# Optimization experiments

Measured on AMD Instinct MI355X. Metric: run time of the kernel, lower is better.

Reference implementation:

```python
import jax, jax.numpy as jnp
import numpy as np

B, F, N = 16, 64, 32768
C0, C1, C2 = 64, 16, 1
TOP_K = 64
EPS = 1e-5


def setup_inputs() -> dict:
    key = jax.random.key(0)
    ks = jax.random.split(key, 6)
    def rn(k, shape, scale=1.0):
        return jax.random.normal(k, shape, dtype=jnp.float32) * scale
    return {
        "sortvec": rn(ks[0], (B, 1, F, N)),
        "input": rn(ks[1], (B, F, N)),
        # conv0: kernel (F,1), in=1, out=64 -> weight reduces to [C0, F]
        "w0": rn(ks[2], (C0, F), np.sqrt(2.0 / F)), "b0": jnp.zeros((C0,), jnp.float32),
        "w1": rn(ks[3], (C1, C0), np.sqrt(2.0 / C0)), "b1": jnp.zeros((C1,), jnp.float32),
        "w2": rn(ks[4], (C2, C1), np.sqrt(2.0 / C1)), "b2": jnp.zeros((C2,), jnp.float32),
        "g0": jnp.ones((C0,), jnp.float32), "bt0": jnp.zeros((C0,), jnp.float32),
        "g1": jnp.ones((C1,), jnp.float32), "bt1": jnp.zeros((C1,), jnp.float32),
        "g2": jnp.ones((C2,), jnp.float32), "bt2": jnp.zeros((C2,), jnp.float32),
    }


def _bn_relu(x, g, b):
    # training-mode BatchNorm2d over (B, N) per channel; x: [B, C, N]
    mu = jnp.mean(x, axis=(0, 2), keepdims=True)
    var = jnp.var(x, axis=(0, 2), keepdims=True)
    return jax.nn.relu((x - mu) * jax.lax.rsqrt(var + EPS) * g[None, :, None] + b[None, :, None])


def reference(sortvec, input, w0, b0, w1, b1, w2, b2, g0, bt0, g1, bt1, g2, bt2):
    # conv0 with kernel (F,1) collapses the feature axis: [B,1,F,N] -> [B,C0,N]
    x = jnp.einsum('bfn,of->bon', sortvec[:, 0], w0) + b0[None, :, None]
    x = _bn_relu(x, g0, bt0)
    x = _bn_relu(jnp.einsum('bcn,oc->bon', x, w1) + b1[None, :, None], g1, bt1)
    score = _bn_relu(jnp.einsum('bcn,oc->bon', x, w2) + b2[None, :, None], g2, bt2)  # [B,1,N]
    _, idx = jax.lax.top_k(score[:, 0], TOP_K)                                        # [B,K]
    sorted_input = jnp.take_along_axis(input, idx[:, None, :], axis=2)                # [B,F,K]
    sorted_score = jnp.take_along_axis(score, idx[:, None, :], axis=2)                # [B,1,K]
    feat = jnp.concatenate([sorted_input, sorted_score], axis=1)                      # [B,F+1,K]
    return feat, idx
```

## Files before the change

### kernel.cpp

```cpp
#include <hip/hip_runtime.h>


constexpr int   B_   = 16;
constexpr int   N_   = 32768;
constexpr int   K_   = 64;
constexpr long long S_ = (long long)B_ * N_;
constexpr float EPS_ = 1e-5f;

constexpr int T128  = 4096;
constexpr int NB0   = 2048;
constexpr int NB1   = 2048;
constexpr int NB2   = 256;
constexpr int NBC   = 128;
constexpr int NBINS = 4096;
constexpr int CAP   = 1024;

__device__ __forceinline__ unsigned key_map(float f) {
  unsigned u = __float_as_uint(f);
  return (u & 0x80000000u) ? ~u : (u | 0x80000000u);
}

__global__ __launch_bounds__(256) void k_prep(const float* __restrict__ w0,
                                              const float* __restrict__ w1,
                                              float* __restrict__ w0T,
                                              float* __restrict__ w1T) {
  int t = threadIdx.x;
  for (int e = t; e < 64 * 64; e += 256) {
    int o = e >> 6, f = e & 63;
    w0T[f * 64 + o] = w0[e];
  }
  for (int e = t; e < 16 * 64; e += 256) {
    int o = e >> 6, c = e & 63;
    w1T[c * 16 + o] = w1[e];
  }
}

__global__ __launch_bounds__(256) void k_stat0(const float* __restrict__ sv,
                                               const float* __restrict__ w0T,
                                               const float* __restrict__ b0,
                                               float* __restrict__ p0) {
  __shared__ float svt[64][128];
  const int t  = threadIdx.x;
  const int p  = t & 63;
  const int cg = __builtin_amdgcn_readfirstlane(t >> 6);

  float bb[16];
#pragma unroll
  for (int j = 0; j < 16; ++j) bb[j] = b0[cg * 16 + j];

  float s1[16], s2[16];
#pragma unroll
  for (int j = 0; j < 16; ++j) { s1[j] = 0.f; s2[j] = 0.f; }

  for (int tile = blockIdx.x; tile < T128; tile += NB0) {
    const int b  = tile >> 8;
    const int n0 = (tile & 255) << 7;
    const float* src = sv + ((long long)b * 64) * N_ + n0;
    __syncthreads();
#pragma unroll
    for (int q = 0; q < 8; ++q) {
      int e = t + q * 256;
      int f = e >> 5, c4 = (e & 31) << 2;
      *(float4*)&svt[f][c4] = *(const float4*)(src + (long long)f * N_ + c4);
    }
    __syncthreads();

    float2 y[16];
#pragma unroll
    for (int j = 0; j < 16; ++j) { y[j].x = bb[j]; y[j].y = bb[j]; }
    for (int f = 0; f < 64; ++f) {
      const float2 x = *(const float2*)&svt[f][p << 1];
      const float* wr = w0T + f * 64 + cg * 16;
#pragma unroll
      for (int j = 0; j < 16; ++j) {
        y[j].x = fmaf(wr[j], x.x, y[j].x);
        y[j].y = fmaf(wr[j], x.y, y[j].y);
      }
    }
#pragma unroll
    for (int j = 0; j < 16; ++j) {
      s1[j] += y[j].x + y[j].y;
      s2[j] = fmaf(y[j].x, y[j].x, fmaf(y[j].y, y[j].y, s2[j]));
    }
  }

#pragma unroll
  for (int j = 0; j < 16; ++j) {
#pragma unroll
    for (int off = 32; off; off >>= 1) {
      s1[j] += __shfl_down(s1[j], off, 64);
      s2[j] += __shfl_down(s2[j], off, 64);
    }
  }
  if (p == 0) {
    float* dst = p0 + (long long)blockIdx.x * 128;
#pragma unroll
    for (int j = 0; j < 16; ++j) {
      dst[cg * 16 + j]      = s1[j];
      dst[64 + cg * 16 + j] = s2[j];
    }
  }
}

__global__ __launch_bounds__(1024) void k_reduce0(const float* __restrict__ p0,
                                                  const float* __restrict__ g,
                                                  const float* __restrict__ bt,
                                                  float* __restrict__ st) {
  __shared__ float l[8][128];
  const int t = threadIdx.x;
  const int j = t & 127, grp = t >> 7;
  float a0 = 0.f, a1 = 0.f, a2 = 0.f, a3 = 0.f;
  for (int i = grp; i < 512; i += 8) {
    a0 += p0[(long long)i * 128 + j];
    a1 += p0[(long long)(i + 512) * 128 + j];
    a2 += p0[(long long)(i + 1024) * 128 + j];
    a3 += p0[(long long)(i + 1536) * 128 + j];
  }
  l[grp][j] = (a0 + a1) + (a2 + a3);
  __syncthreads();
  if (t < 128) {
    float v = ((l[0][t] + l[1][t]) + (l[2][t] + l[3][t])) +
              ((l[4][t] + l[5][t]) + (l[6][t] + l[7][t]));
    l[0][t] = v;
  }
  __syncthreads();
  if (t < 64) {
    const float inv = 1.f / (float)S_;
    float mean = l[0][t] * inv;
    float ex2  = l[0][64 + t] * inv;
    float var  = ex2 - mean * mean;
    float sc   = g[t] * rsqrtf(var + EPS_);
    st[t]      = sc;
    st[64 + t] = bt[t] - mean * sc;
  }
}

__global__ __launch_bounds__(256) void k_layer01(const float* __restrict__ sv,
                                                 const float* __restrict__ w0T,
                                                 const float* __restrict__ b0,
                                                 const float* __restrict__ st0,
                                                 const float* __restrict__ w1T,
                                                 const float* __restrict__ b1,
                                                 float* __restrict__ y1,
                                                 float* __restrict__ p1) {
  __shared__ float buf[64][128];
  const int t  = threadIdx.x;
  const int p  = t & 63;
  const int cg = __builtin_amdgcn_readfirstlane(t >> 6);

  float bb[16], sc[16], sh[16];
#pragma unroll
  for (int j = 0; j < 16; ++j) {
    bb[j] = b0[cg * 16 + j];
    sc[j] = st0[cg * 16 + j];
    sh[j] = st0[64 + cg * 16 + j];
  }
  float bb1[4];
#pragma unroll
  for (int j = 0; j < 4; ++j) bb1[j] = b1[cg * 4 + j];

  float sA[4], qA[4];
#pragma unroll
  for (int j = 0; j < 4; ++j) { sA[j] = 0.f; qA[j] = 0.f; }

  for (int tile = blockIdx.x; tile < T128; tile += NB1) {
    const int b  = tile >> 8;
    const int n0 = (tile & 255) << 7;
    const float* src = sv + ((long long)b * 64) * N_ + n0;
    __syncthreads();
#pragma unroll
    for (int q = 0; q < 8; ++q) {
      int e = t + q * 256;
      int f = e >> 5, c4 = (e & 31) << 2;
      *(float4*)&buf[f][c4] = *(const float4*)(src + (long long)f * N_ + c4);
    }
    __syncthreads();

    float2 y[16];
#pragma unroll
    for (int j = 0; j < 16; ++j) { y[j].x = bb[j]; y[j].y = bb[j]; }
    for (int f = 0; f < 64; ++f) {
      const float2 x = *(const float2*)&buf[f][p << 1];
      const float* wr = w0T + f * 64 + cg * 16;
#pragma unroll
      for (int j = 0; j < 16; ++j) {
        y[j].x = fmaf(wr[j], x.x, y[j].x);
        y[j].y = fmaf(wr[j], x.y, y[j].y);
      }
    }
    __syncthreads();

#pragma unroll
    for (int j = 0; j < 16; ++j) {
      float2 h;
      h.x = fmaf(y[j].x, sc[j], sh[j]); h.x = h.x > 0.f ? h.x : 0.f;
      h.y = fmaf(y[j].y, sc[j], sh[j]); h.y = h.y > 0.f ? h.y : 0.f;
      *(float2*)&buf[cg * 16 + j][p << 1] = h;
    }
    __syncthreads();

    float2 z[4];
#pragma unroll
    for (int j = 0; j < 4; ++j) { z[j].x = bb1[j]; z[j].y = bb1[j]; }
    for (int c = 0; c < 64; ++c) {
      const float2 h = *(const float2*)&buf[c][p << 1];
      const float* wr = w1T + c * 16 + cg * 4;
#pragma unroll
      for (int j = 0; j < 4; ++j) {
        z[j].x = fmaf(wr[j], h.x, z[j].x);
        z[j].y = fmaf(wr[j], h.y, z[j].y);
      }
    }

    float* yo = y1 + ((long long)(b * 16 + cg * 4)) * N_ + n0 + (p << 1);
#pragma unroll
    for (int j = 0; j < 4; ++j) {
      *(float2*)(yo + (long long)j * N_) = z[j];
      sA[j] += z[j].x + z[j].y;
      qA[j] = fmaf(z[j].x, z[j].x, fmaf(z[j].y, z[j].y, qA[j]));
    }
  }

#pragma unroll
  for (int j = 0; j < 4; ++j) {
#pragma unroll
    for (int off = 32; off; off >>= 1) {
      sA[j] += __shfl_down(sA[j], off, 64);
      qA[j] += __shfl_down(qA[j], off, 64);
    }
  }
  if (p == 0) {
    float* dst = p1 + (long long)blockIdx.x * 32;
#pragma unroll
    for (int j = 0; j < 4; ++j) {
      dst[cg * 4 + j]      = sA[j];
      dst[16 + cg * 4 + j] = qA[j];
    }
  }
}

__global__ __launch_bounds__(1024) void k_reduce1(const float* __restrict__ p1,
                                                  const float* __restrict__ g,
                                                  const float* __restrict__ bt,
                                                  float* __restrict__ st) {
  __shared__ float l[32][32];
  const int t = threadIdx.x;
  const int j = t & 31, grp = t >> 5;
  float a0 = 0.f, a1 = 0.f;
  for (int i = grp; i < 1024; i += 32) {
    a0 += p1[(long long)i * 32 + j];
    a1 += p1[(long long)(i + 1024) * 32 + j];
  }
  l[grp][j] = a0 + a1;
  __syncthreads();
  if (t < 32) {
    float v = 0.f;
#pragma unroll
    for (int g2 = 0; g2 < 32; ++g2) v += l[g2][t];
    l[0][t] = v;
  }
  __syncthreads();
  if (t < 16) {
    const float inv = 1.f / (float)S_;
    float mean = l[0][t] * inv;
    float ex2  = l[0][16 + t] * inv;
    float var  = ex2 - mean * mean;
    float sc   = g[t] * rsqrtf(var + EPS_);
    st[t]      = sc;
    st[16 + t] = bt[t] - mean * sc;
  }
}

__global__ __launch_bounds__(1024) void k_layer2(const float* __restrict__ y1,
                                                 const float* __restrict__ st1,
                                                 const float* __restrict__ w2,
                                                 const float* __restrict__ b2,
                                                 float* __restrict__ y2,
                                                 float* __restrict__ p2,
                                                 int* __restrict__ ghist) {
  __shared__ int hist[NBINS];
  __shared__ float ls[16], lq[16];
  const int t   = threadIdx.x;
  const int blk = blockIdx.x;
  const int b   = blk >> 4;
  const int n0  = ((blk & 15) << 11) | (t << 1);

#pragma unroll
  for (int i = 0; i < NBINS / 1024; ++i) hist[t + i * 1024] = 0;

  float sc[16], sh[16], w[16];
#pragma unroll
  for (int c = 0; c < 16; ++c) { sc[c] = st1[c]; sh[c] = st1[16 + c]; w[c] = w2[c]; }
  const float bias = b2[0];

  float a0 = bias, a1 = bias;
  const float* base = y1 + ((long long)b * 16) * N_ + n0;
#pragma unroll
  for (int c = 0; c < 16; ++c) {
    float2 v = *(const float2*)(base + (long long)c * N_);
    float h;
    h = fmaf(v.x, sc[c], sh[c]); h = h > 0.f ? h : 0.f; a0 = fmaf(w[c], h, a0);
    h = fmaf(v.y, sc[c], sh[c]); h = h > 0.f ? h : 0.f; a1 = fmaf(w[c], h, a1);
  }
  float2 o; o.x = a0; o.y = a1;
  *(float2*)(y2 + (long long)b * N_ + n0) = o;

  __syncthreads();

  atomicAdd(&hist[key_map(a0) >> 20], 1);
  atomicAdd(&hist[key_map(a1) >> 20], 1);

  float ss = a0 + a1;
  float sq = fmaf(a0, a0, a1 * a1);
#pragma unroll
  for (int off = 32; off; off >>= 1) {
    ss += __shfl_down(ss, off, 64);
    sq += __shfl_down(sq, off, 64);
  }
  const int wid = t >> 6, lid = t & 63;
  if (lid == 0) { ls[wid] = ss; lq[wid] = sq; }
  __syncthreads();
  if (t == 0) {
    float Sv = 0.f, Qv = 0.f;
#pragma unroll
    for (int i = 0; i < 16; ++i) { Sv += ls[i]; Qv += lq[i]; }
    p2[blk * 2 + 0] = Sv;
    p2[blk * 2 + 1] = Qv;
  }
#pragma unroll
  for (int i = 0; i < NBINS / 1024; ++i) {
    int v = hist[t + i * 1024];
    if (v) atomicAdd(&ghist[b * NBINS + t + i * 1024], v);
  }
}

__global__ __launch_bounds__(256) void k_thresh(const int* __restrict__ ghist,
                                                int* __restrict__ Tb) {
  __shared__ int hl[NBINS + NBINS / 64];
  const int t = threadIdx.x, b = blockIdx.x;
  const int* h = ghist + b * NBINS;
  for (int i = t; i < NBINS; i += 256) hl[i + (i >> 6)] = h[i];
  __syncthreads();
  if (t < 64) {
    const int l = t;
    int s = 0;
    for (int j = 0; j < 64; ++j) s += hl[(l * 64 + j) + l];
    int Sv = s;
#pragma unroll
    for (int off = 1; off < 64; off <<= 1) {
      int v = __shfl_down(Sv, off, 64);
      if (l + off < 64) Sv += v;
    }
    unsigned long long m = __ballot(Sv >= K_);
    const int lstar = 63 - __builtin_clzll(m);
    const int tailS = (lstar < 63) ? __shfl(Sv, lstar + 1, 64) : 0;
    int Tj = hl[(lstar * 64 + l) + lstar];
#pragma unroll
    for (int off = 1; off < 64; off <<= 1) {
      int v = __shfl_down(Tj, off, 64);
      if (l + off < 64) Tj += v;
    }
    const int cge = Tj + tailS;
    unsigned long long m2 = __ballot(cge >= K_);
    const int jstar = 63 - __builtin_clzll(m2);
    if (l == 0) Tb[b] = lstar * 64 + jstar;
  }
}

__global__ __launch_bounds__(1024) void k_compact(const float* __restrict__ y2,
                                                  const int* __restrict__ Tb,
                                                  int* __restrict__ cnt,
                                                  unsigned long long* __restrict__ cand) {
  const int t = threadIdx.x, blk = blockIdx.x;
  const int b  = blk >> 3;
  const int n0 = ((blk & 7) << 12) | (t << 2);
  const int T  = Tb[b];
  float4 v = *(const float4*)(y2 + (long long)b * N_ + n0);
  unsigned long long* cb = cand + (long long)b * CAP;
#define DO_CAND(comp, off)                                                    \
  {                                                                           \
    unsigned u = key_map(comp);                                               \
    if ((int)(u >> 20) >= T) {                                                \
      int slot = atomicAdd(&cnt[b], 1);                                       \
      if (slot < CAP)                                                         \
        cb[slot] = ((unsigned long long)u << 32) |                            \
                   (unsigned)(N_ - 1 - (n0 + off));                           \
    }                                                                         \
  }
  DO_CAND(v.x, 0) DO_CAND(v.y, 1) DO_CAND(v.z, 2) DO_CAND(v.w, 3)
#undef DO_CAND
}

__global__ __launch_bounds__(64) void k_final(const unsigned long long* __restrict__ cand,
                                              const int* __restrict__ cnt,
                                              const float* __restrict__ p2,
                                              const float* __restrict__ g2,
                                              const float* __restrict__ bt2,
                                              const float* __restrict__ inp,
                                              float* __restrict__ out) {
  const int b = blockIdx.x, l = threadIdx.x;

  float s1 = (p2[2 * l] + p2[2 * (l + 64)]) +
             (p2[2 * (l + 128)] + p2[2 * (l + 192)]);
  float q1 = (p2[2 * l + 1] + p2[2 * (l + 64) + 1]) +
             (p2[2 * (l + 128) + 1] + p2[2 * (l + 192) + 1]);
#pragma unroll
  for (int off = 32; off; off >>= 1) {
    s1 += __shfl_down(s1, off, 64);
    q1 += __shfl_down(q1, off, 64);
  }
  s1 = __shfl(s1, 0, 64);
  q1 = __shfl(q1, 0, 64);
  const float inv = 1.f / (float)S_;
  const float mean = s1 * inv;
  const float var  = q1 * inv - mean * mean;
  const float scale2 = g2[0] * rsqrtf(var + EPS_);
  const float shift2 = bt2[0] - mean * scale2;

  int cn = cnt[b];
  if (cn > CAP) cn = CAP;
  const unsigned long long* cb = cand + (long long)b * CAP;
  unsigned long long k[16];
#pragma unroll
  for (int r = 0; r < 16; ++r) {
    int i = l + r * 64;
    k[r] = (i < cn) ? cb[i] : 0ull;
  }
  unsigned long long cur = 0ull;
#pragma unroll
  for (int r = 0; r < 16; ++r) cur = k[r] > cur ? k[r] : cur;

  int myidx = 0;
  unsigned mymap = 0;
  for (int r = 0; r < K_; ++r) {
    unsigned long long m = cur;
#pragma unroll
    for (int off = 32; off; off >>= 1) {
      unsigned long long o = __shfl_xor(m, off, 64);
      m = o > m ? o : m;
    }
    if (r == l) {
      myidx = N_ - 1 - (int)(m & 0xffffffffu);
      mymap = (unsigned)(m >> 32);
    }
    if (cur == m) {
#pragma unroll
      for (int r2 = 0; r2 < 16; ++r2)
        if (k[r2] == m) k[r2] = 0ull;
      unsigned long long c2 = 0ull;
#pragma unroll
      for (int r2 = 0; r2 < 16; ++r2) c2 = k[r2] > c2 ? k[r2] : c2;
      cur = c2;
    }
  }

  unsigned u = mymap;
  u = (u & 0x80000000u) ? (u & 0x7fffffffu) : ~u;
  float v = __uint_as_float(u);
  float scv = fmaf(v, scale2, shift2);
  scv = scv > 0.f ? scv : 0.f;

  const float* ib = inp + ((long long)b * 64) * N_;
#pragma unroll 4
  for (int f = 0; f < 64; ++f)
    out[((long long)b * 65 + f) * 64 + l] = ib[(long long)f * N_ + myidx];
  out[((long long)b * 65 + 64) * 64 + l] = scv;
  out[(long long)B_ * 65 * 64 + b * 64 + l] = (float)myidx;
}

extern "C" void kernel_launch(void* const* d_in, const int* in_sizes, int n_in,
                              void* d_out, int out_size, void* d_ws, size_t ws_size,
                              hipStream_t stream) {
  const float* sv  = (const float*)d_in[0];
  const float* inp = (const float*)d_in[1];
  const float* w0  = (const float*)d_in[2];
  const float* b0  = (const float*)d_in[3];
  const float* w1  = (const float*)d_in[4];
  const float* b1  = (const float*)d_in[5];
  const float* w2  = (const float*)d_in[6];
  const float* b2  = (const float*)d_in[7];
  const float* g0  = (const float*)d_in[8];
  const float* bt0 = (const float*)d_in[9];
  const float* g1  = (const float*)d_in[10];
  const float* bt1 = (const float*)d_in[11];
  const float* g2  = (const float*)d_in[12];
  const float* bt2 = (const float*)d_in[13];
  float* out = (float*)d_out;

  float* ws  = (float*)d_ws;
  float* y1  = ws;
  float* y2  = y1 + (size_t)S_ * 16;
  float* p0  = y2 + (size_t)S_;
  float* p1  = p0 + (size_t)NB0 * 128;
  float* p2  = p1 + (size_t)NB1 * 32;
  float* st0 = p2 + (size_t)NB2 * 2;
  float* st1 = st0 + 128;
  float* w0T = st1 + 32;
  float* w1T = w0T + 4096;
  int*   ghist = (int*)(w1T + 1024);
  int*   cnt   = ghist + (size_t)B_ * NBINS;
  int*   Tb    = cnt + 16;
  unsigned long long* cand =
      (unsigned long long*)(Tb + 16);

  hipMemsetAsync(ghist, 0, ((size_t)B_ * NBINS + 16) * sizeof(int), stream);

  k_prep   <<<1,    256, 0, stream>>>(w0, w1, w0T, w1T);
  k_stat0  <<<NB0,  256, 0, stream>>>(sv, w0T, b0, p0);
  k_reduce0<<<1,   1024, 0, stream>>>(p0, g0, bt0, st0);
  k_layer01<<<NB1,  256, 0, stream>>>(sv, w0T, b0, st0, w1T, b1, y1, p1);
  k_reduce1<<<1,   1024, 0, stream>>>(p1, g1, bt1, st1);
  k_layer2 <<<NB2, 1024, 0, stream>>>(y1, st1, w2, b2, y2, p2, ghist);
  k_thresh <<<B_,   256, 0, stream>>>(ghist, Tb);
  k_compact<<<NBC, 1024, 0, stream>>>(y2, Tb, cnt, cand);
  k_final  <<<B_,    64, 0, stream>>>(cand, cnt, p2, g2, bt2, inp, out);
}
```

Baseline: 292.8 us.

## Double-buffer tiles via global_load_lds, restructure layer1, fuse selection kernels

Switches the conv tile staging in k_stat0 and k_layer01 to 64-column tiles that are double-buffered through direct global-to-LDS loads, so the next tile's load overlaps the current tile's compute. Layer1 now computes partial 16x16 products per channel group in registers and reduces them through shared memory. The old LDS round trip of the full hidden activation is gone, at the cost of an extra shared buffer. The histogram memset moves into k_stat0, and the threshold, compaction and final top-k kernels merge into one per-batch k_select that keeps candidates in LDS. This removes launches and global atomics, but only 16 blocks now scan y2.

Result: no change. 291.1 us (-0.6%).

```diff
diff --git a/kernel.cpp b/kernel.cpp
--- a/kernel.cpp
+++ b/kernel.cpp
@@ -7,11 +7,9 @@
 constexpr long long S_ = (long long)B_ * N_;
 constexpr float EPS_ = 1e-5f;
 
-constexpr int T128  = 4096;
 constexpr int NB0   = 2048;
 constexpr int NB1   = 2048;
 constexpr int NB2   = 256;
-constexpr int NBC   = 128;
 constexpr int NBINS = 4096;
 constexpr int CAP   = 1024;
 
@@ -20,29 +18,49 @@
   return (u & 0x80000000u) ? ~u : (u | 0x80000000u);
 }
 
+__device__ __forceinline__ void gload16(const float* g, float* l) {
+  __builtin_amdgcn_global_load_lds(
+      (const __attribute__((address_space(1))) void*)g,
+      (__attribute__((address_space(3))) void*)l, 16, 0, 0);
+}
+
+__device__ __forceinline__ void stage_tile(const float* __restrict__ src,
+                                           float (*dst)[64], int t) {
+#pragma unroll
+  for (int q = 0; q < 4; ++q) {
+    const int e = t + q * 256;
+    const int f = e >> 4, c4 = (e & 15) << 2;
+    gload16(src + (long long)f * N_ + c4, &dst[f][c4]);
+  }
+}
+
 __global__ __launch_bounds__(256) void k_prep(const float* __restrict__ w0,
                                               const float* __restrict__ w1,
                                               float* __restrict__ w0T,
-                                              float* __restrict__ w1T) {
+                                              float* __restrict__ w1p) {
   int t = threadIdx.x;
   for (int e = t; e < 64 * 64; e += 256) {
     int o = e >> 6, f = e & 63;
     w0T[f * 64 + o] = w0[e];
   }
   for (int e = t; e < 16 * 64; e += 256) {
-    int o = e >> 6, c = e & 63;
-    w1T[c * 16 + o] = w1[e];
+    int cg = e >> 8, rem = e & 255, o = rem >> 4, j = rem & 15;
+    w1p[e] = w1[o * 64 + cg * 16 + j];
   }
 }
 
 __global__ __launch_bounds__(256) void k_stat0(const float* __restrict__ sv,
                                                const float* __restrict__ w0T,
                                                const float* __restrict__ b0,
-                                               float* __restrict__ p0) {
-  __shared__ float svt[64][128];
-  const int t  = threadIdx.x;
-  const int p  = t & 63;
-  const int cg = __builtin_amdgcn_readfirstlane(t >> 6);
+                                               float* __restrict__ p0,
+                                               int* __restrict__ ghist) {
+  __shared__ float svt[2][64][64];
+  const int t   = threadIdx.x;
+  const int p   = t & 63;
+  const int cg  = __builtin_amdgcn_readfirstlane(t >> 6);
+  const int bid = blockIdx.x;
+
+  if (t < 32) ghist[bid * 32 + t] = 0;
 
   float bb[16];
 #pragma unroll
@@ -52,36 +70,35 @@
 #pragma unroll
   for (int j = 0; j < 16; ++j) { s1[j] = 0.f; s2[j] = 0.f; }
 
-  for (int tile = blockIdx.x; tile < T128; tile += NB0) {
-    const int b  = tile >> 8;
-    const int n0 = (tile & 255) << 7;
-    const float* src = sv + ((long long)b * 64) * N_ + n0;
+  {
+    const int tile = bid;
+    const int b = tile >> 9, n0 = (tile & 511) << 6;
+    stage_tile(sv + ((long long)b * 64) * N_ + n0, svt[0], t);
+  }
+  int cur = 0;
+#pragma unroll
+  for (int i = 0; i < 4; ++i) {
     __syncthreads();
-#pragma unroll
-    for (int q = 0; q < 8; ++q) {
-      int e = t + q * 256;
-      int f = e >> 5, c4 = (e & 31) << 2;
-      *(float4*)&svt[f][c4] = *(const float4*)(src + (long long)f * N_ + c4);
-    }
-    __syncthreads();
-
-    float2 y[16];
-#pragma unroll
-    for (int j = 0; j < 16; ++j) { y[j].x = bb[j]; y[j].y = bb[j]; }
+    if (i + 1 < 4) {
+      const int tile = bid + (i + 1) * NB0;
+      const int b = tile >> 9, n0 = (tile & 511) << 6;
+      stage_tile(sv + ((long long)b * 64) * N_ + n0, svt[cur ^ 1], t);
+    }
+    float y[16];
+#pragma unroll
+    for (int j = 0; j < 16; ++j) y[j] = bb[j];
     for (int f = 0; f < 64; ++f) {
-      const float2 x = *(const float2*)&svt[f][p << 1];
+      const float x = svt[cur][f][p];
       const float* wr = w0T + f * 64 + cg * 16;
 #pragma unroll
-      for (int j = 0; j < 16; ++j) {
-        y[j].x = fmaf(wr[j], x.x, y[j].x);
-        y[j].y = fmaf(wr[j], x.y, y[j].y);
-      }
+      for (int j = 0; j < 16; ++j) y[j] = fmaf(wr[j], x, y[j]);
     }
 #pragma unroll
     for (int j = 0; j < 16; ++j) {
-      s1[j] += y[j].x + y[j].y;
-      s2[j] = fmaf(y[j].x, y[j].x, fmaf(y[j].y, y[j].y, s2[j]));
-    }
+      s1[j] += y[j];
+      s2[j] = fmaf(y[j], y[j], s2[j]);
+    }
+    cur ^= 1;
   }
 
 #pragma unroll
@@ -93,7 +110,7 @@
     }
   }
   if (p == 0) {
-    float* dst = p0 + (long long)blockIdx.x * 128;
+    float* dst = p0 + (long long)bid * 128;
 #pragma unroll
     for (int j = 0; j < 16; ++j) {
       dst[cg * 16 + j]      = s1[j];
@@ -109,14 +126,9 @@
   __shared__ float l[8][128];
   const int t = threadIdx.x;
   const int j = t & 127, grp = t >> 7;
-  float a0 = 0.f, a1 = 0.f, a2 = 0.f, a3 = 0.f;
-  for (int i = grp; i < 512; i += 8) {
-    a0 += p0[(long long)i * 128 + j];
-    a1 += p0[(long long)(i + 512) * 128 + j];
-    a2 += p0[(long long)(i + 1024) * 128 + j];
-    a3 += p0[(long long)(i + 1536) * 128 + j];
-  }
-  l[grp][j] = (a0 + a1) + (a2 + a3);
+  float a = 0.f;
+  for (int i = grp; i < NB0; i += 8) a += p0[(long long)i * 128 + j];
+  l[grp][j] = a;
   __syncthreads();
   if (t < 128) {
     float v = ((l[0][t] + l[1][t]) + (l[2][t] + l[3][t])) +
@@ -139,14 +151,16 @@
                                                  const float* __restrict__ w0T,
                                                  const float* __restrict__ b0,
                                                  const float* __restrict__ st0,
-                                                 const float* __restrict__ w1T,
+                                                 const float* __restrict__ w1p,
                                                  const float* __restrict__ b1,
                                                  float* __restrict__ y1,
                                                  float* __restrict__ p1) {
-  __shared__ float buf[64][128];
-  const int t  = threadIdx.x;
-  const int p  = t & 63;
-  const int cg = __builtin_amdgcn_readfirstlane(t >> 6);
+  __shared__ float svt[2][64][64];
+  __shared__ float zp[4][16][64];
+  const int t   = threadIdx.x;
+  const int p   = t & 63;
+  const int cg  = __builtin_amdgcn_readfirstlane(t >> 6);
+  const int bid = blockIdx.x;
 
   float bb[16], sc[16], sh[16];
 #pragma unroll
@@ -163,62 +177,59 @@
 #pragma unroll
   for (int j = 0; j < 4; ++j) { sA[j] = 0.f; qA[j] = 0.f; }
 
-  for (int tile = blockIdx.x; tile < T128; tile += NB1) {
-    const int b  = tile >> 8;
-    const int n0 = (tile & 255) << 7;
-    const float* src = sv + ((long long)b * 64) * N_ + n0;
+  {
+    const int tile = bid;
+    const int b = tile >> 9, n0 = (tile & 511) << 6;
+    stage_tile(sv + ((long long)b * 64) * N_ + n0, svt[0], t);
+  }
+  int cur = 0;
+#pragma unroll
+  for (int i = 0; i < 4; ++i) {
+    const int tile = bid + i * NB0;
+    const int b = tile >> 9, n0 = (tile & 511) << 6;
+
     __syncthreads();
-#pragma unroll
-    for (int q = 0; q < 8; ++q) {
-      int e = t + q * 256;
-      int f = e >> 5, c4 = (e & 31) << 2;
-      *(float4*)&buf[f][c4] = *(const float4*)(src + (long long)f * N_ + c4);
+    if (i + 1 < 4) {
+      const int tile2 = bid + (i + 1) * NB0;
+      const int b2 = tile2 >> 9, n02 = (tile2 & 511) << 6;
+      stage_tile(sv + ((long long)b2 * 64) * N_ + n02, svt[cur ^ 1], t);
+    }
+
+    float y[16];
+#pragma unroll
+    for (int j = 0; j < 16; ++j) y[j] = bb[j];
+    for (int f = 0; f < 64; ++f) {
+      const float x = svt[cur][f][p];
+      const float* wr = w0T + f * 64 + cg * 16;
+#pragma unroll
+      for (int j = 0; j < 16; ++j) y[j] = fmaf(wr[j], x, y[j]);
+    }
+#pragma unroll
+    for (int j = 0; j < 16; ++j) {
+      float h = fmaf(y[j], sc[j], sh[j]);
+      y[j] = h > 0.f ? h : 0.f;
+    }
+    const float* wp = w1p + cg * 256;
+#pragma unroll
+    for (int o = 0; o < 16; ++o) {
+      float acc = 0.f;
+#pragma unroll
+      for (int j = 0; j < 16; ++j) acc = fmaf(wp[o * 16 + j], y[j], acc);
+      zp[cg][o][p] = acc;
     }
     __syncthreads();
 
-    float2 y[16];
-#pragma unroll
-    for (int j = 0; j < 16; ++j) { y[j].x = bb[j]; y[j].y = bb[j]; }
-    for (int f = 0; f < 64; ++f) {
-      const float2 x = *(const float2*)&buf[f][p << 1];
-      const float* wr = w0T + f * 64 + cg * 16;
-#pragma unroll
-      for (int j = 0; j < 16; ++j) {
-        y[j].x = fmaf(wr[j], x.x, y[j].x);
-        y[j].y = fmaf(wr[j], x.y, y[j].y);
-      }
-    }
-    __syncthreads();
-
-#pragma unroll
-    for (int j = 0; j < 16; ++j) {
-      float2 h;
-      h.x = fmaf(y[j].x, sc[j], sh[j]); h.x = h.x > 0.f ? h.x : 0.f;
-      h.y = fmaf(y[j].y, sc[j], sh[j]); h.y = h.y > 0.f ? h.y : 0.f;
-      *(float2*)&buf[cg * 16 + j][p << 1] = h;
-    }
-    __syncthreads();
-
-    float2 z[4];
-#pragma unroll
-    for (int j = 0; j < 4; ++j) { z[j].x = bb1[j]; z[j].y = bb1[j]; }
-    for (int c = 0; c < 64; ++c) {
-      const float2 h = *(const float2*)&buf[c][p << 1];
-      const float* wr = w1T + c * 16 + cg * 4;
-#pragma unroll
-      for (int j = 0; j < 4; ++j) {
-        z[j].x = fmaf(wr[j], h.x, z[j].x);
-        z[j].y = fmaf(wr[j], h.y, z[j].y);
-      }
-    }
-
-    float* yo = y1 + ((long long)(b * 16 + cg * 4)) * N_ + n0 + (p << 1);
-#pragma unroll
-    for (int j = 0; j < 4; ++j) {
-      *(float2*)(yo + (long long)j * N_) = z[j];
-      sA[j] += z[j].x + z[j].y;
-      qA[j] = fmaf(z[j].x, z[j].x, fmaf(z[j].y, z[j].y, qA[j]));
-    }
+    float* yo = y1 + ((long long)(b * 16 + cg * 4)) * N_ + n0 + p;
+#pragma unroll
+    for (int oi = 0; oi < 4; ++oi) {
+      const int o = cg * 4 + oi;
+      float z = ((zp[0][o][p] + zp[1][o][p]) +
+                 (zp[2][o][p] + zp[3][o][p])) + bb1[oi];
+      yo[(long long)oi * N_] = z;
+      sA[oi] += z;
+      qA[oi] = fmaf(z, z, qA[oi]);
+    }
+    cur ^= 1;
   }
 
 #pragma unroll
@@ -230,7 +241,7 @@
     }
   }
   if (p == 0) {
-    float* dst = p1 + (long long)blockIdx.x * 32;
+    float* dst = p1 + (long long)bid * 32;
 #pragma unroll
     for (int j = 0; j < 4; ++j) {
       dst[cg * 4 + j]      = sA[j];
@@ -246,12 +257,9 @@
   __shared__ float l[32][32];
   const int t = threadIdx.x;
   const int j = t & 31, grp = t >> 5;
-  float a0 = 0.f, a1 = 0.f;
-  for (int i = grp; i < 1024; i += 32) {
-    a0 += p1[(long long)i * 32 + j];
-    a1 += p1[(long long)(i + 1024) * 32 + j];
-  }
-  l[grp][j] = a0 + a1;
+  float a = 0.f;
+  for (int i = grp; i < NB1; i += 32) a += p1[(long long)i * 32 + j];
+  l[grp][j] = a;
   __syncthreads();
   if (t < 32) {
     float v = 0.f;
@@ -334,13 +342,40 @@
   }
 }
 
-__global__ __launch_bounds__(256) void k_thresh(const int* __restrict__ ghist,
-                                                int* __restrict__ Tb) {
+__global__ __launch_bounds__(1024) void k_select(const float* __restrict__ y2,
+                                                 const int* __restrict__ ghist,
+                                                 const float* __restrict__ p2,
+                                                 const float* __restrict__ g2,
+                                                 const float* __restrict__ bt2,
+                                                 const float* __restrict__ inp,
+                                                 float* __restrict__ out) {
   __shared__ int hl[NBINS + NBINS / 64];
+  __shared__ float sred[512];
+  __shared__ unsigned long long cand[CAP];
+  __shared__ int lcnt;
+  __shared__ int sT;
+  __shared__ float s2v[2];
+  __shared__ int   idxs[K_];
+  __shared__ float scores[K_];
+
   const int t = threadIdx.x, b = blockIdx.x;
   const int* h = ghist + b * NBINS;
-  for (int i = t; i < NBINS; i += 256) hl[i + (i >> 6)] = h[i];
-  __syncthreads();
+  for (int i = t; i < NBINS; i += 1024) hl[i + (i >> 6)] = h[i];
+  if (t < 512) sred[t] = p2[t];
+  if (t == 0) lcnt = 0;
+  __syncthreads();
+  for (int s = 256; s >= 2; s >>= 1) {
+    if (t < s) sred[t] += sred[t + s];
+    __syncthreads();
+  }
+  if (t == 0) {
+    const float inv = 1.f / (float)S_;
+    float mean = sred[0] * inv;
+    float var  = sred[1] * inv - mean * mean;
+    float scv  = g2[0] * rsqrtf(var + EPS_);
+    s2v[0] = scv;
+    s2v[1] = bt2[0] - mean * scv;
+  }
   if (t < 64) {
     const int l = t;
     int s = 0;
@@ -363,109 +398,83 @@
     const int cge = Tj + tailS;
     unsigned long long m2 = __ballot(cge >= K_);
     const int jstar = 63 - __builtin_clzll(m2);
-    if (l == 0) Tb[b] = lstar * 64 + jstar;
-  }
-}
-
-__global__ __launch_bounds__(1024) void k_compact(const float* __restrict__ y2,
-                                                  const int* __restrict__ Tb,
-                                                  int* __restrict__ cnt,
-                                                  unsigned long long* __restrict__ cand) {
-  const int t = threadIdx.x, blk = blockIdx.x;
-  const int b  = blk >> 3;
-  const int n0 = ((blk & 7) << 12) | (t << 2);
-  const int T  = Tb[b];
-  float4 v = *(const float4*)(y2 + (long long)b * N_ + n0);
-  unsigned long long* cb = cand + (long long)b * CAP;
+    if (l == 0) sT = lstar * 64 + jstar;
+  }
+  __syncthreads();
+
+  const int T = sT;
+  const float* yrow = y2 + (long long)b * N_;
+  for (int it = 0; it < 8; ++it) {
+    const int n0 = (it << 12) | (t << 2);
+    float4 v = *(const float4*)(yrow + n0);
 #define DO_CAND(comp, off)                                                    \
-  {                                                                           \
-    unsigned u = key_map(comp);                                               \
-    if ((int)(u >> 20) >= T) {                                                \
-      int slot = atomicAdd(&cnt[b], 1);                                       \
-      if (slot < CAP)                                                         \
-        cb[slot] = ((unsigned long long)u << 32) |                            \
-                   (unsigned)(N_ - 1 - (n0 + off));                           \
-    }                                                                         \
-  }
-  DO_CAND(v.x, 0) DO_CAND(v.y, 1) DO_CAND(v.z, 2) DO_CAND(v.w, 3)
+    {                                                                         \
+      unsigned u = key_map(comp);                                             \
+      if ((int)(u >> 20) >= T) {                                              \
+        int slot = atomicAdd(&lcnt, 1);                                       \
+        if (slot < CAP)                                                       \
+          cand[slot] = ((unsigned long long)u << 32) |                        \
+                       (unsigned)(N_ - 1 - (n0 + off));                       \
+      }                                                                       \
+    }
+    DO_CAND(v.x, 0) DO_CAND(v.y, 1) DO_CAND(v.z, 2) DO_CAND(v.w, 3)
 #undef DO_CAND
-}
-
-__global__ __launch_bounds__(64) void k_final(const unsigned long long* __restrict__ cand,
-                                              const int* __restrict__ cnt,
-                                              const float* __restrict__ p2,
-                                              const float* __restrict__ g2,
-                                              const float* __restrict__ bt2,
-                                              const float* __restrict__ inp,
-                                              float* __restrict__ out) {
-  const int b = blockIdx.x, l = threadIdx.x;
-
-  float s1 = (p2[2 * l] + p2[2 * (l + 64)]) +
-             (p2[2 * (l + 128)] + p2[2 * (l + 192)]);
-  float q1 = (p2[2 * l + 1] + p2[2 * (l + 64) + 1]) +
-             (p2[2 * (l + 128) + 1] + p2[2 * (l + 192) + 1]);
-#pragma unroll
-  for (int off = 32; off; off >>= 1) {
-    s1 += __shfl_down(s1, off, 64);
-    q1 += __shfl_down(q1, off, 64);
-  }
-  s1 = __shfl(s1, 0, 64);
-  q1 = __shfl(q1, 0, 64);
-  const float inv = 1.f / (float)S_;
-  const float mean = s1 * inv;
-  const float var  = q1 * inv - mean * mean;
-  const float scale2 = g2[0] * rsqrtf(var + EPS_);
-  const float shift2 = bt2[0] - mean * scale2;
-
-  int cn = cnt[b];
-  if (cn > CAP) cn = CAP;
-  const unsigned long long* cb = cand + (long long)b * CAP;
-  unsigned long long k[16];
-#pragma unroll
-  for (int r = 0; r < 16; ++r) {
-    int i = l + r * 64;
-    k[r] = (i < cn) ? cb[i] : 0ull;
-  }
-  unsigned long long cur = 0ull;
-#pragma unroll
-  for (int r = 0; r < 16; ++r) cur = k[r] > cur ? k[r] : cur;
-
-  int myidx = 0;
-  unsigned mymap = 0;
-  for (int r = 0; r < K_; ++r) {
-    unsigned long long m = cur;
-#pragma unroll
-    for (int off = 32; off; off >>= 1) {
-      unsigned long long o = __shfl_xor(m, off, 64);
-      m = o > m ? o : m;
-    }
-    if (r == l) {
-      myidx = N_ - 1 - (int)(m & 0xffffffffu);
-      mymap = (unsigned)(m >> 32);
-    }
-    if (cur == m) {
-#pragma unroll
-      for (int r2 = 0; r2 < 16; ++r2)
-        if (k[r2] == m) k[r2] = 0ull;
-      unsigned long long c2 = 0ull;
-#pragma unroll
-      for (int r2 = 0; r2 < 16; ++r2) c2 = k[r2] > c2 ? k[r2] : c2;
-      cur = c2;
-    }
-  }
-
-  unsigned u = mymap;
-  u = (u & 0x80000000u) ? (u & 0x7fffffffu) : ~u;
-  float v = __uint_as_float(u);
-  float scv = fmaf(v, scale2, shift2);
-  scv = scv > 0.f ? scv : 0.f;
+  }
+  __syncthreads();
+
+  if (t < 64) {
+    const int l = t;
+    int cn = lcnt;
+    if (cn > CAP) cn = CAP;
+    unsigned long long k[16];
+#pragma unroll
+    for (int r = 0; r < 16; ++r) {
+      int i = l + r * 64;
+      k[r] = (i < cn) ? cand[i] : 0ull;
+    }
+    unsigned long long curk = 0ull;
+#pragma unroll
+    for (int r = 0; r < 16; ++r) curk = k[r] > curk ? k[r] : curk;
+
+    int myidx = 0;
+    unsigned mymap = 0;
+    for (int r = 0; r < K_; ++r) {
+      unsigned long long m = curk;
+#pragma unroll
+      for (int off = 32; off; off >>= 1) {
+        unsigned long long o = __shfl_xor(m, off, 64);
+        m = o > m ? o : m;
+      }
+      if (r == l) {
+        myidx = N_ - 1 - (int)(m & 0xffffffffu);
+        mymap = (unsigned)(m >> 32);
+      }
+      if (curk == m) {
+#pragma unroll
+        for (int r2 = 0; r2 < 16; ++r2)
+          if (k[r2] == m) k[r2] = 0ull;
+        unsigned long long c2 = 0ull;
+#pragma unroll
+        for (int r2 = 0; r2 < 16; ++r2) c2 = k[r2] > c2 ? k[r2] : c2;
+        curk = c2;
+      }
+    }
+    unsigned u = mymap;
+    u = (u & 0x80000000u) ? (u & 0x7fffffffu) : ~u;
+    float v = __uint_as_float(u);
+    float scv = fmaf(v, s2v[0], s2v[1]);
+    scores[l] = scv > 0.f ? scv : 0.f;
+    idxs[l]   = myidx;
+  }
+  __syncthreads();
 
   const float* ib = inp + ((long long)b * 64) * N_;
-#pragma unroll 4
-  for (int f = 0; f < 64; ++f)
-    out[((long long)b * 65 + f) * 64 + l] = ib[(long long)f * N_ + myidx];
-  out[((long long)b * 65 + 64) * 64 + l] = scv;
-  out[(long long)B_ * 65 * 64 + b * 64 + l] = (float)myidx;
+  for (int e = t; e < 65 * 64; e += 1024) {
+    const int f = e >> 6, k = e & 63;
+    out[((long long)b * 65 + f) * 64 + k] =
+        (f < 64) ? ib[(long long)f * N_ + idxs[k]] : scores[k];
+  }
+  if (t < K_) out[(long long)B_ * 65 * 64 + b * 64 + t] = (float)idxs[t];
 }
 
 extern "C" void kernel_launch(void* const* d_in, const int* in_sizes, int n_in,
@@ -493,25 +502,17 @@
   float* p0  = y2 + (size_t)S_;
   float* p1  = p0 + (size_t)NB0 * 128;
   float* p2  = p1 + (size_t)NB1 * 32;
-  float* st0 = p2 + (size_t)NB2 * 2;
+  float* st0 = p2 + 512;
   float* st1 = st0 + 128;
   float* w0T = st1 + 32;
-  float* w1T = w0T + 4096;
-  int*   ghist = (int*)(w1T + 1024);
-  int*   cnt   = ghist + (size_t)B_ * NBINS;
-  int*   Tb    = cnt + 16;
-  unsigned long long* cand =
-      (unsigned long long*)(Tb + 16);
-
-  hipMemsetAsync(ghist, 0, ((size_t)B_ * NBINS + 16) * sizeof(int), stream);
-
-  k_prep   <<<1,    256, 0, stream>>>(w0, w1, w0T, w1T);
-  k_stat0  <<<NB0,  256, 0, stream>>>(sv, w0T, b0, p0);
-  k_reduce0<<<1,   1024, 0, stream>>>(p0, g0, bt0, st0);
-  k_layer01<<<NB1,  256, 0, stream>>>(sv, w0T, b0, st0, w1T, b1, y1, p1);
-  k_reduce1<<<1,   1024, 0, stream>>>(p1, g1, bt1, st1);
-  k_layer2 <<<NB2, 1024, 0, stream>>>(y1, st1, w2, b2, y2, p2, ghist);
-  k_thresh <<<B_,   256, 0, stream>>>(ghist, Tb);
-  k_compact<<<NBC, 1024, 0, stream>>>(y2, Tb, cnt, cand);
-  k_final  <<<B_,    64, 0, stream>>>(cand, cnt, p2, g2, bt2, inp, out);
-}
+  float* w1p = w0T + 4096;
+  int*   ghist = (int*)(w1p + 1024);
+
+  k_prep   <<<1,     256, 0, stream>>>(w0, w1, w0T, w1p);
+  k_stat0  <<<NB0,   256, 0, stream>>>(sv, w0T, b0, p0, ghist);
+  k_reduce0<<<1,    1024, 0, stream>>>(p0, g0, bt0, st0);
+  k_layer01<<<NB1,   256, 0, stream>>>(sv, w0T, b0, st0, w1p, b1, y1, p1);
+  k_reduce1<<<1,    1024, 0, stream>>>(p1, g1, bt1, st1);
+  k_layer2 <<<NB2,  1024, 0, stream>>>(y1, st1, w2, b2, y2, p2, ghist);
+  k_select <<<B_,   1024, 0, stream>>>(y2, ghist, p2, g2, bt2, inp, out);
+}
```
